# Kernel optimization log

Hardware: AMD Instinct MI355X
Metric: run time of the kernel (lower is better)

## Reference

```python
import jax, jax.numpy as jnp
import numpy as np

N = 50000
E = 1_600_000
HID = 128
NF = 128
NG = 64
CUTOFF = 10.0
LOG2 = float(np.log(2.0))
PI = float(np.pi)


def ssp(v):
    # ShiftedSoftplus: softplus(v) - log(2), numerically stable
    return jnp.logaddexp(v, 0.0) - LOG2


def setup_inputs() -> dict:
    key = jax.random.key(0)
    ks = jax.random.split(key, 12)
    s = 0.05
    x = jax.random.normal(ks[0], (N, HID), dtype=jnp.float32)
    edge_index = jax.random.randint(ks[1], (2, E), 0, N, dtype=jnp.int64 if jax.config.jax_enable_x64 else jnp.int32)
    edge_length = jax.random.uniform(ks[2], (E,), dtype=jnp.float32) * 12.0
    edge_attr = jax.random.normal(ks[3], (E, NG), dtype=jnp.float32)
    return {
        "x": x,
        "edge_index": edge_index,
        "edge_length": edge_length,
        "edge_attr": edge_attr,
        "lin1_w": jax.random.normal(ks[4], (HID, NF), dtype=jnp.float32) * s,
        "nn_w1": jax.random.normal(ks[5], (NG, NF), dtype=jnp.float32) * s,
        "nn_b1": jnp.zeros((NF,), dtype=jnp.float32),
        "nn_w2": jax.random.normal(ks[6], (NF, NF), dtype=jnp.float32) * s,
        "nn_b2": jnp.zeros((NF,), dtype=jnp.float32),
        "lin2_w": jax.random.normal(ks[7], (NF, HID), dtype=jnp.float32) * s,
        "lin2_b": jnp.zeros((HID,), dtype=jnp.float32),
        "lin_w": jax.random.normal(ks[8], (HID, HID), dtype=jnp.float32) * s,
        "lin_b": jnp.zeros((HID,), dtype=jnp.float32),
    }


def reference(x, edge_index, edge_length, edge_attr,
              lin1_w, nn_w1, nn_b1, nn_w2, nn_b2,
              lin2_w, lin2_b, lin_w, lin_b):
    # edge filter MLP: [E, NG] -> [E, NF]
    W = ssp(edge_attr @ nn_w1 + nn_b1) @ nn_w2 + nn_b2
    # cosine cutoff envelope
    C = 0.5 * (jnp.cos(edge_length * (PI / CUTOFF)) + 1.0)
    C = C * (edge_length <= CUTOFF) * (edge_length >= 0.0)
    W = W * C[:, None]
    # node projection, gather source, multiply, scatter-add to target
    h = x @ lin1_w                                   # [N, NF]
    src, dst = edge_index[0], edge_index[1]
    msg = h[src] * W                                 # [E, NF]
    agg = jax.ops.segment_sum(msg, dst, num_segments=N)  # [N, NF]
    out = agg @ lin2_w + lin2_b                      # [N, HID]
    out = ssp(out)
    out = out @ lin_w + lin_b
    return out
```

## Files before the change

kernel.cpp:

```cpp
#include <hip/hip_runtime.h>


typedef __attribute__((ext_vector_type(8))) short bf16x8;
typedef __attribute__((ext_vector_type(4))) float f32x4;

static __device__ __forceinline__ float sspf(float v) {
    return fmaxf(v, 0.0f) + __logf(1.0f + __expf(-fabsf(v))) - 0.69314718f;
}

static __device__ __forceinline__ short bf16s(float x) {
    unsigned u = __builtin_bit_cast(unsigned, x);
    return (short)((u + 0x7fffu + ((u >> 16) & 1u)) >> 16);
}

__global__ __launch_bounds__(256) void node_proj_kernel(
    const float* __restrict__ x, const float* __restrict__ w,
    float* __restrict__ h, int n)
{
    __shared__ float xsT[128 * 20];
    int row0 = blockIdx.x * 16;
    for (int i = threadIdx.x; i < 2048; i += 256) {
        int r = i >> 7, c = i & 127;
        int rr = row0 + r;
        xsT[c * 20 + r] = (rr < n) ? x[(size_t)rr * 128 + c] : 0.0f;
    }
    __syncthreads();
    int j = threadIdx.x & 127;
    int rb = (threadIdx.x >> 7) * 8;
    float acc[8] = {0, 0, 0, 0, 0, 0, 0, 0};
    for (int k = 0; k < 128; ++k) {
        float wk = w[k * 128 + j];
        const float4* xp = (const float4*)&xsT[k * 20 + rb];
        float4 u0 = xp[0], u1 = xp[1];
        acc[0] = fmaf(u0.x, wk, acc[0]);
        acc[1] = fmaf(u0.y, wk, acc[1]);
        acc[2] = fmaf(u0.z, wk, acc[2]);
        acc[3] = fmaf(u0.w, wk, acc[3]);
        acc[4] = fmaf(u1.x, wk, acc[4]);
        acc[5] = fmaf(u1.y, wk, acc[5]);
        acc[6] = fmaf(u1.z, wk, acc[6]);
        acc[7] = fmaf(u1.w, wk, acc[7]);
    }
#pragma unroll
    for (int r = 0; r < 8; ++r) {
        int rr = row0 + rb + r;
        if (rr < n) h[(size_t)rr * 128 + j] = acc[r];
    }
}

__global__ __launch_bounds__(512, 4) void edge_kernel(
    const float* __restrict__ eattr, const int* __restrict__ eidx,
    const float* __restrict__ elen,
    const float* __restrict__ w1, const float* __restrict__ b1,
    const float* __restrict__ w2, const float* __restrict__ b2,
    const float* __restrict__ h, float* __restrict__ agg, int E)
{
    __shared__ short w1T[128 * 72];
    __shared__ short w2T[128 * 136];
    __shared__ short tseg[8 * 16 * 40];

    for (int i = threadIdx.x; i < 64 * 128; i += 512) {
        int k = i >> 7, nn = i & 127;
        w1T[nn * 72 + k] = bf16s(w1[i]);
    }
    for (int i = threadIdx.x; i < 128 * 128; i += 512) {
        int k = i >> 7, nn = i & 127;
        w2T[nn * 136 + k] = bf16s(w2[i]);
    }
    __syncthreads();

    const int lane = threadIdx.x & 63;
    const int m = lane & 15;
    const int q = lane >> 4;
    short* tw = tseg + (threadIdx.x >> 6) * (16 * 40);

    float b1v[8], b2v[8];
#pragma unroll
    for (int u = 0; u < 8; ++u) {
        b1v[u] = b1[u * 16 + m];
        b2v[u] = b2[u * 16 + m];
    }

    const int ngroups = (E + 15) >> 4;
    int wid = blockIdx.x * 8 + (threadIdx.x >> 6);
    int stride = gridDim.x * 8;

    for (int g = wid; g < ngroups; g += stride) {
        int e0 = g << 4;

        int erow = e0 + m;
        if (erow >= E) erow = E - 1;
        const float* ap = eattr + (size_t)erow * 64 + q * 8;
        float4 x0 = *(const float4*)(ap);
        float4 x1 = *(const float4*)(ap + 4);
        float4 x2 = *(const float4*)(ap + 32);
        float4 x3 = *(const float4*)(ap + 36);
        bf16x8 af0, af1;
        af0[0] = bf16s(x0.x); af0[1] = bf16s(x0.y);
        af0[2] = bf16s(x0.z); af0[3] = bf16s(x0.w);
        af0[4] = bf16s(x1.x); af0[5] = bf16s(x1.y);
        af0[6] = bf16s(x1.z); af0[7] = bf16s(x1.w);
        af1[0] = bf16s(x2.x); af1[1] = bf16s(x2.y);
        af1[2] = bf16s(x2.z); af1[3] = bf16s(x2.w);
        af1[4] = bf16s(x3.x); af1[5] = bf16s(x3.y);
        af1[6] = bf16s(x3.z); af1[7] = bf16s(x3.w);

        float cvv[4];
        int sV[4], dV[4];
#pragma unroll
        for (int r = 0; r < 4; ++r) {
            int e = e0 + 4 * q + r;
            int ec = (e < E) ? e : 0;
            float len = elen[ec];
            sV[r] = eidx[ec];
            dV[r] = eidx[E + ec];
            bool ok = (e < E) && (len <= 10.0f) && (len >= 0.0f);
            cvv[r] = ok ? 0.5f * (__cosf(len * 0.31415927f) + 1.0f) : 0.0f;
        }

        f32x4 acc2[8];
#pragma unroll
        for (int nt = 0; nt < 8; ++nt) {
            f32x4 c; c[0] = b2v[nt]; c[1] = b2v[nt]; c[2] = b2v[nt]; c[3] = b2v[nt];
            acc2[nt] = c;
        }

#pragma unroll
        for (int k2 = 0; k2 < 4; ++k2) {
            f32x4 acc1[2];
#pragma unroll
            for (int t = 0; t < 2; ++t) {
                float bv = b1v[2 * k2 + t];
                f32x4 c; c[0] = bv; c[1] = bv; c[2] = bv; c[3] = bv;
                acc1[t] = c;
            }
#pragma unroll
            for (int t = 0; t < 2; ++t) {
#pragma unroll
                for (int a = 0; a < 2; ++a) {
                    bf16x8 bw = *(const bf16x8*)&w1T[(16 * (2 * k2 + t) + m) * 72 + a * 32 + q * 8];
                    acc1[t] = __builtin_amdgcn_mfma_f32_16x16x32_bf16(
                        (a == 0) ? af0 : af1, bw, acc1[t], 0, 0, 0);
                }
            }
#pragma unroll
            for (int t = 0; t < 2; ++t) {
#pragma unroll
                for (int r = 0; r < 4; ++r) {
                    tw[(4 * q + r) * 40 + 16 * t + m] = bf16s(sspf(acc1[t][r]));
                }
            }
            bf16x8 ta = *(const bf16x8*)&tw[m * 40 + q * 8];
#pragma unroll
            for (int nt = 0; nt < 8; ++nt) {
                bf16x8 bw2 = *(const bf16x8*)&w2T[(16 * nt + m) * 136 + k2 * 32 + q * 8];
                acc2[nt] = __builtin_amdgcn_mfma_f32_16x16x32_bf16(ta, bw2, acc2[nt], 0, 0, 0);
            }
        }

#pragma unroll
        for (int r = 0; r < 4; ++r) {
            float cv = cvv[r];
            if (cv != 0.0f) {
                const float* hp = h + (size_t)sV[r] * 128 + m;
                float* gp = agg + (size_t)dV[r] * 128 + m;
#pragma unroll
                for (int nt = 0; nt < 8; ++nt) {
                    float Wv = acc2[nt][r] * cv;
                    atomicAdd(gp + nt * 16, hp[nt * 16] * Wv);
                }
            }
        }
    }
}

__global__ __launch_bounds__(256) void out_kernel(
    const float* __restrict__ agg,
    const float* __restrict__ w2, const float* __restrict__ b2,
    const float* __restrict__ w3, const float* __restrict__ b3,
    float* __restrict__ out, int n)
{
    __shared__ float aT[128 * 20];
    __shared__ float mT[128 * 20];
    int row0 = blockIdx.x * 16;
    for (int i = threadIdx.x; i < 2048; i += 256) {
        int r = i >> 7, c = i & 127;
        int rr = row0 + r;
        aT[c * 20 + r] = (rr < n) ? agg[(size_t)rr * 128 + c] : 0.0f;
    }
    __syncthreads();
    int j = threadIdx.x & 127;
    int rb = (threadIdx.x >> 7) * 8;

    float acc[8];
    float bj = b2[j];
#pragma unroll
    for (int r = 0; r < 8; ++r) acc[r] = bj;
    for (int k = 0; k < 128; ++k) {
        float wk = w2[k * 128 + j];
        const float4* xp = (const float4*)&aT[k * 20 + rb];
        float4 u0 = xp[0], u1 = xp[1];
        acc[0] = fmaf(u0.x, wk, acc[0]);
        acc[1] = fmaf(u0.y, wk, acc[1]);
        acc[2] = fmaf(u0.z, wk, acc[2]);
        acc[3] = fmaf(u0.w, wk, acc[3]);
        acc[4] = fmaf(u1.x, wk, acc[4]);
        acc[5] = fmaf(u1.y, wk, acc[5]);
        acc[6] = fmaf(u1.z, wk, acc[6]);
        acc[7] = fmaf(u1.w, wk, acc[7]);
    }
    float4 s0, s1;
    s0.x = sspf(acc[0]); s0.y = sspf(acc[1]); s0.z = sspf(acc[2]); s0.w = sspf(acc[3]);
    s1.x = sspf(acc[4]); s1.y = sspf(acc[5]); s1.z = sspf(acc[6]); s1.w = sspf(acc[7]);
    ((float4*)&mT[j * 20 + rb])[0] = s0;
    ((float4*)&mT[j * 20 + rb])[1] = s1;
    __syncthreads();

    float bj3 = b3[j];
#pragma unroll
    for (int r = 0; r < 8; ++r) acc[r] = bj3;
    for (int k = 0; k < 128; ++k) {
        float wk = w3[k * 128 + j];
        const float4* xp = (const float4*)&mT[k * 20 + rb];
        float4 u0 = xp[0], u1 = xp[1];
        acc[0] = fmaf(u0.x, wk, acc[0]);
        acc[1] = fmaf(u0.y, wk, acc[1]);
        acc[2] = fmaf(u0.z, wk, acc[2]);
        acc[3] = fmaf(u0.w, wk, acc[3]);
        acc[4] = fmaf(u1.x, wk, acc[4]);
        acc[5] = fmaf(u1.y, wk, acc[5]);
        acc[6] = fmaf(u1.z, wk, acc[6]);
        acc[7] = fmaf(u1.w, wk, acc[7]);
    }
#pragma unroll
    for (int r = 0; r < 8; ++r) {
        int rr = row0 + rb + r;
        if (rr < n) out[(size_t)rr * 128 + j] = acc[r];
    }
}

extern "C" void kernel_launch(void* const* d_in, const int* in_sizes, int n_in,
                              void* d_out, int out_size, void* d_ws, size_t ws_size,
                              hipStream_t stream)
{
    const float* x     = (const float*)d_in[0];
    const int*   eidx  = (const int*)d_in[1];
    const float* elen  = (const float*)d_in[2];
    const float* eattr = (const float*)d_in[3];
    const float* lin1w = (const float*)d_in[4];
    const float* nnw1  = (const float*)d_in[5];
    const float* nnb1  = (const float*)d_in[6];
    const float* nnw2  = (const float*)d_in[7];
    const float* nnb2  = (const float*)d_in[8];
    const float* lin2w = (const float*)d_in[9];
    const float* lin2b = (const float*)d_in[10];
    const float* linw  = (const float*)d_in[11];
    const float* linb  = (const float*)d_in[12];

    int n = in_sizes[0] / 128;
    int E = in_sizes[2];

    float* h   = (float*)d_ws;
    float* agg = h + (size_t)n * 128;

    hipMemsetAsync(agg, 0, (size_t)n * 128 * sizeof(float), stream);

    node_proj_kernel<<<(n + 15) / 16, 256, 0, stream>>>(x, lin1w, h, n);
    edge_kernel<<<512, 512, 0, stream>>>(eattr, eidx, elen,
                                         nnw1, nnb1, nnw2, nnb2, h, agg, E);
    out_kernel<<<(n + 15) / 16, 256, 0, stream>>>(agg, lin2w, lin2b, linw, linb,
                                                  (float*)d_out, n);
}
```

Measured before the change: 1.248 ms.

## Transpose first edge MFMA and pass activations via shuffles instead of LDS

The first filter MFMA is swapped to compute the transposed tile, so the ssp activations can be packed to bf16 pairs and redistributed with wave shuffles. This replaces the per-wave LDS staging buffer. Biases move to shared memory and b2 is added at the scatter stage, which frees registers; occupancy is raised to 6 blocks of 512 with a 768-block grid. The node and output GEMM kernels also change their thread-to-column mapping to two columns by four rows. The extra shuffles and selects add ALU work, and the higher occupancy target may force register spills.

```diff
diff --git a/kernel.cpp b/kernel.cpp
--- a/kernel.cpp
+++ b/kernel.cpp
@@ -11,6 +11,10 @@
 static __device__ __forceinline__ short bf16s(float x) {
     unsigned u = __builtin_bit_cast(unsigned, x);
     return (short)((u + 0x7fffu + ((u >> 16) & 1u)) >> 16);
+}
+static __device__ __forceinline__ int packbf(float lo, float hi) {
+    return (int)(((unsigned)(unsigned short)bf16s(lo)) |
+                 (((unsigned)(unsigned short)bf16s(hi)) << 16));
 }
 
 __global__ __launch_bounds__(256) void node_proj_kernel(
@@ -25,30 +29,33 @@
         xsT[c * 20 + r] = (rr < n) ? x[(size_t)rr * 128 + c] : 0.0f;
     }
     __syncthreads();
-    int j = threadIdx.x & 127;
-    int rb = (threadIdx.x >> 7) * 8;
+    int c0 = threadIdx.x & 63, c1 = c0 + 64;
+    int rg = threadIdx.x >> 6;
     float acc[8] = {0, 0, 0, 0, 0, 0, 0, 0};
     for (int k = 0; k < 128; ++k) {
-        float wk = w[k * 128 + j];
-        const float4* xp = (const float4*)&xsT[k * 20 + rb];
-        float4 u0 = xp[0], u1 = xp[1];
-        acc[0] = fmaf(u0.x, wk, acc[0]);
-        acc[1] = fmaf(u0.y, wk, acc[1]);
-        acc[2] = fmaf(u0.z, wk, acc[2]);
-        acc[3] = fmaf(u0.w, wk, acc[3]);
-        acc[4] = fmaf(u1.x, wk, acc[4]);
-        acc[5] = fmaf(u1.y, wk, acc[5]);
-        acc[6] = fmaf(u1.z, wk, acc[6]);
-        acc[7] = fmaf(u1.w, wk, acc[7]);
-    }
-#pragma unroll
-    for (int r = 0; r < 8; ++r) {
-        int rr = row0 + rb + r;
-        if (rr < n) h[(size_t)rr * 128 + j] = acc[r];
-    }
-}
-
-__global__ __launch_bounds__(512, 4) void edge_kernel(
+        float4 xv = *(const float4*)&xsT[k * 20 + 4 * rg];
+        float w0 = w[k * 128 + c0];
+        float w1v = w[k * 128 + c1];
+        acc[0] = fmaf(xv.x, w0, acc[0]);
+        acc[1] = fmaf(xv.y, w0, acc[1]);
+        acc[2] = fmaf(xv.z, w0, acc[2]);
+        acc[3] = fmaf(xv.w, w0, acc[3]);
+        acc[4] = fmaf(xv.x, w1v, acc[4]);
+        acc[5] = fmaf(xv.y, w1v, acc[5]);
+        acc[6] = fmaf(xv.z, w1v, acc[6]);
+        acc[7] = fmaf(xv.w, w1v, acc[7]);
+    }
+#pragma unroll
+    for (int r = 0; r < 4; ++r) {
+        int rr = row0 + 4 * rg + r;
+        if (rr < n) {
+            h[(size_t)rr * 128 + c0] = acc[r];
+            h[(size_t)rr * 128 + c1] = acc[4 + r];
+        }
+    }
+}
+
+__global__ __launch_bounds__(512, 6) void edge_kernel(
     const float* __restrict__ eattr, const int* __restrict__ eidx,
     const float* __restrict__ elen,
     const float* __restrict__ w1, const float* __restrict__ b1,
@@ -57,29 +64,30 @@
 {
     __shared__ short w1T[128 * 72];
     __shared__ short w2T[128 * 136];
-    __shared__ short tseg[8 * 16 * 40];
+    __shared__ float b1s[128];
+    __shared__ float b2s[128];
 
     for (int i = threadIdx.x; i < 64 * 128; i += 512) {
-        int k = i >> 7, nn = i & 127;
-        w1T[nn * 72 + k] = bf16s(w1[i]);
+        int k = i >> 7, c = i & 127;
+        w1T[c * 72 + k] = bf16s(w1[i]);
     }
     for (int i = threadIdx.x; i < 128 * 128; i += 512) {
-        int k = i >> 7, nn = i & 127;
-        w2T[nn * 136 + k] = bf16s(w2[i]);
+        int k = i >> 7, c = i & 127;
+        w2T[c * 136 + k] = bf16s(w2[i]);
+    }
+    if (threadIdx.x < 128) {
+        b1s[threadIdx.x] = b1[threadIdx.x];
+        b2s[threadIdx.x] = b2[threadIdx.x];
     }
     __syncthreads();
 
     const int lane = threadIdx.x & 63;
     const int m = lane & 15;
     const int q = lane >> 4;
-    short* tw = tseg + (threadIdx.x >> 6) * (16 * 40);
-
-    float b1v[8], b2v[8];
-#pragma unroll
-    for (int u = 0; u < 8; ++u) {
-        b1v[u] = b1[u * 16 + m];
-        b2v[u] = b2[u * 16 + m];
-    }
+    const int s_ = q & 1;
+    const int L0 = 32 * s_ + m;
+    const int L1 = L0 + 16;
+    const bool hiTile = (q >= 2);
 
     const int ngroups = (E + 15) >> 4;
     int wid = blockIdx.x * 8 + (threadIdx.x >> 6);
@@ -105,6 +113,49 @@
         af1[4] = bf16s(x3.x); af1[5] = bf16s(x3.y);
         af1[6] = bf16s(x3.z); af1[7] = bf16s(x3.w);
 
+        f32x4 acc2[8];
+#pragma unroll
+        for (int nt = 0; nt < 8; ++nt) {
+            f32x4 z; z[0] = 0.f; z[1] = 0.f; z[2] = 0.f; z[3] = 0.f;
+            acc2[nt] = z;
+        }
+
+#pragma unroll
+        for (int kc = 0; kc < 4; ++kc) {
+            int pk[4];
+#pragma unroll
+            for (int t = 0; t < 2; ++t) {
+                int ct2 = 2 * kc + t;
+                f32x4 a1; a1[0] = 0.f; a1[1] = 0.f; a1[2] = 0.f; a1[3] = 0.f;
+                bf16x8 wA0 = *(const bf16x8*)&w1T[(16 * ct2 + m) * 72 + 8 * q];
+                bf16x8 wA1 = *(const bf16x8*)&w1T[(16 * ct2 + m) * 72 + 32 + 8 * q];
+                a1 = __builtin_amdgcn_mfma_f32_16x16x32_bf16(wA0, af0, a1, 0, 0, 0);
+                a1 = __builtin_amdgcn_mfma_f32_16x16x32_bf16(wA1, af1, a1, 0, 0, 0);
+                float4 bb = *(const float4*)&b1s[16 * ct2 + 4 * q];
+                float v0 = sspf(a1[0] + bb.x);
+                float v1 = sspf(a1[1] + bb.y);
+                float v2 = sspf(a1[2] + bb.z);
+                float v3 = sspf(a1[3] + bb.w);
+                pk[2 * t]     = packbf(v0, v1);
+                pk[2 * t + 1] = packbf(v2, v3);
+            }
+            int fa0 = __shfl(pk[0], L0), fa1 = __shfl(pk[1], L0);
+            int fa2 = __shfl(pk[0], L1), fa3 = __shfl(pk[1], L1);
+            int fb0 = __shfl(pk[2], L0), fb1 = __shfl(pk[3], L0);
+            int fb2 = __shfl(pk[2], L1), fb3 = __shfl(pk[3], L1);
+            int4 fr;
+            fr.x = hiTile ? fb0 : fa0;
+            fr.y = hiTile ? fb1 : fa1;
+            fr.z = hiTile ? fb2 : fa2;
+            fr.w = hiTile ? fb3 : fa3;
+            bf16x8 ta = __builtin_bit_cast(bf16x8, fr);
+#pragma unroll
+            for (int nt = 0; nt < 8; ++nt) {
+                bf16x8 bw2 = *(const bf16x8*)&w2T[(16 * nt + m) * 136 + 32 * kc + 8 * q];
+                acc2[nt] = __builtin_amdgcn_mfma_f32_16x16x32_bf16(ta, bw2, acc2[nt], 0, 0, 0);
+            }
+        }
+
         float cvv[4];
         int sV[4], dV[4];
 #pragma unroll
@@ -117,46 +168,9 @@
             bool ok = (e < E) && (len <= 10.0f) && (len >= 0.0f);
             cvv[r] = ok ? 0.5f * (__cosf(len * 0.31415927f) + 1.0f) : 0.0f;
         }
-
-        f32x4 acc2[8];
-#pragma unroll
-        for (int nt = 0; nt < 8; ++nt) {
-            f32x4 c; c[0] = b2v[nt]; c[1] = b2v[nt]; c[2] = b2v[nt]; c[3] = b2v[nt];
-            acc2[nt] = c;
-        }
-
-#pragma unroll
-        for (int k2 = 0; k2 < 4; ++k2) {
-            f32x4 acc1[2];
-#pragma unroll
-            for (int t = 0; t < 2; ++t) {
-                float bv = b1v[2 * k2 + t];
-                f32x4 c; c[0] = bv; c[1] = bv; c[2] = bv; c[3] = bv;
-                acc1[t] = c;
-            }
-#pragma unroll
-            for (int t = 0; t < 2; ++t) {
-#pragma unroll
-                for (int a = 0; a < 2; ++a) {
-                    bf16x8 bw = *(const bf16x8*)&w1T[(16 * (2 * k2 + t) + m) * 72 + a * 32 + q * 8];
-                    acc1[t] = __builtin_amdgcn_mfma_f32_16x16x32_bf16(
-                        (a == 0) ? af0 : af1, bw, acc1[t], 0, 0, 0);
-                }
-            }
-#pragma unroll
-            for (int t = 0; t < 2; ++t) {
-#pragma unroll
-                for (int r = 0; r < 4; ++r) {
-                    tw[(4 * q + r) * 40 + 16 * t + m] = bf16s(sspf(acc1[t][r]));
-                }
-            }
-            bf16x8 ta = *(const bf16x8*)&tw[m * 40 + q * 8];
-#pragma unroll
-            for (int nt = 0; nt < 8; ++nt) {
-                bf16x8 bw2 = *(const bf16x8*)&w2T[(16 * nt + m) * 136 + k2 * 32 + q * 8];
-                acc2[nt] = __builtin_amdgcn_mfma_f32_16x16x32_bf16(ta, bw2, acc2[nt], 0, 0, 0);
-            }
-        }
+        float b2l[8];
+#pragma unroll
+        for (int nt = 0; nt < 8; ++nt) b2l[nt] = b2s[16 * nt + m];
 
 #pragma unroll
         for (int r = 0; r < 4; ++r) {
@@ -166,7 +180,7 @@
                 float* gp = agg + (size_t)dV[r] * 128 + m;
 #pragma unroll
                 for (int nt = 0; nt < 8; ++nt) {
-                    float Wv = acc2[nt][r] * cv;
+                    float Wv = (acc2[nt][r] + b2l[nt]) * cv;
                     atomicAdd(gp + nt * 16, hp[nt * 16] * Wv);
                 }
             }
@@ -189,53 +203,56 @@
         aT[c * 20 + r] = (rr < n) ? agg[(size_t)rr * 128 + c] : 0.0f;
     }
     __syncthreads();
-    int j = threadIdx.x & 127;
-    int rb = (threadIdx.x >> 7) * 8;
+    int c0 = threadIdx.x & 63, c1 = c0 + 64;
+    int rg = threadIdx.x >> 6;
 
     float acc[8];
-    float bj = b2[j];
-#pragma unroll
-    for (int r = 0; r < 8; ++r) acc[r] = bj;
+    float b0 = b2[c0], b1v = b2[c1];
+#pragma unroll
+    for (int r = 0; r < 4; ++r) { acc[r] = b0; acc[4 + r] = b1v; }
     for (int k = 0; k < 128; ++k) {
-        float wk = w2[k * 128 + j];
-        const float4* xp = (const float4*)&aT[k * 20 + rb];
-        float4 u0 = xp[0], u1 = xp[1];
-        acc[0] = fmaf(u0.x, wk, acc[0]);
-        acc[1] = fmaf(u0.y, wk, acc[1]);
-        acc[2] = fmaf(u0.z, wk, acc[2]);
-        acc[3] = fmaf(u0.w, wk, acc[3]);
-        acc[4] = fmaf(u1.x, wk, acc[4]);
-        acc[5] = fmaf(u1.y, wk, acc[5]);
-        acc[6] = fmaf(u1.z, wk, acc[6]);
-        acc[7] = fmaf(u1.w, wk, acc[7]);
+        float4 xv = *(const float4*)&aT[k * 20 + 4 * rg];
+        float w0 = w2[k * 128 + c0];
+        float w1v = w2[k * 128 + c1];
+        acc[0] = fmaf(xv.x, w0, acc[0]);
+        acc[1] = fmaf(xv.y, w0, acc[1]);
+        acc[2] = fmaf(xv.z, w0, acc[2]);
+        acc[3] = fmaf(xv.w, w0, acc[3]);
+        acc[4] = fmaf(xv.x, w1v, acc[4]);
+        acc[5] = fmaf(xv.y, w1v, acc[5]);
+        acc[6] = fmaf(xv.z, w1v, acc[6]);
+        acc[7] = fmaf(xv.w, w1v, acc[7]);
     }
     float4 s0, s1;
     s0.x = sspf(acc[0]); s0.y = sspf(acc[1]); s0.z = sspf(acc[2]); s0.w = sspf(acc[3]);
     s1.x = sspf(acc[4]); s1.y = sspf(acc[5]); s1.z = sspf(acc[6]); s1.w = sspf(acc[7]);
-    ((float4*)&mT[j * 20 + rb])[0] = s0;
-    ((float4*)&mT[j * 20 + rb])[1] = s1;
-    __syncthreads();
-
-    float bj3 = b3[j];
-#pragma unroll
-    for (int r = 0; r < 8; ++r) acc[r] = bj3;
+    *(float4*)&mT[c0 * 20 + 4 * rg] = s0;
+    *(float4*)&mT[c1 * 20 + 4 * rg] = s1;
+    __syncthreads();
+
+    float b30 = b3[c0], b31 = b3[c1];
+#pragma unroll
+    for (int r = 0; r < 4; ++r) { acc[r] = b30; acc[4 + r] = b31; }
     for (int k = 0; k < 128; ++k) {
-        float wk = w3[k * 128 + j];
-        const float4* xp = (const float4*)&mT[k * 20 + rb];
-        float4 u0 = xp[0], u1 = xp[1];
-        acc[0] = fmaf(u0.x, wk, acc[0]);
-        acc[1] = fmaf(u0.y, wk, acc[1]);
-        acc[2] = fmaf(u0.z, wk, acc[2]);
-        acc[3] = fmaf(u0.w, wk, acc[3]);
-        acc[4] = fmaf(u1.x, wk, acc[4]);
-        acc[5] = fmaf(u1.y, wk, acc[5]);
-        acc[6] = fmaf(u1.z, wk, acc[6]);
-        acc[7] = fmaf(u1.w, wk, acc[7]);
-    }
-#pragma unroll
-    for (int r = 0; r < 8; ++r) {
-        int rr = row0 + rb + r;
-        if (rr < n) out[(size_t)rr * 128 + j] = acc[r];
+        float4 xv = *(const float4*)&mT[k * 20 + 4 * rg];
+        float w0 = w3[k * 128 + c0];
+        float w1v = w3[k * 128 + c1];
+        acc[0] = fmaf(xv.x, w0, acc[0]);
+        acc[1] = fmaf(xv.y, w0, acc[1]);
+        acc[2] = fmaf(xv.z, w0, acc[2]);
+        acc[3] = fmaf(xv.w, w0, acc[3]);
+        acc[4] = fmaf(xv.x, w1v, acc[4]);
+        acc[5] = fmaf(xv.y, w1v, acc[5]);
+        acc[6] = fmaf(xv.z, w1v, acc[6]);
+        acc[7] = fmaf(xv.w, w1v, acc[7]);
+    }
+#pragma unroll
+    for (int r = 0; r < 4; ++r) {
+        int rr = row0 + 4 * rg + r;
+        if (rr < n) {
+            out[(size_t)rr * 128 + c0] = acc[r];
+            out[(size_t)rr * 128 + c1] = acc[4 + r];
+        }
     }
 }
 
@@ -266,7 +283,7 @@
     hipMemsetAsync(agg, 0, (size_t)n * 128 * sizeof(float), stream);
 
     node_proj_kernel<<<(n + 15) / 16, 256, 0, stream>>>(x, lin1w, h, n);
-    edge_kernel<<<512, 512, 0, stream>>>(eattr, eidx, elen,
+    edge_kernel<<<768, 512, 0, stream>>>(eattr, eidx, elen,
                                          nnw1, nnb1, nnw2, nnb2, h, agg, E);
     out_kernel<<<(n + 15) / 16, 256, 0, stream>>>(agg, lin2w, lin2b, linw, linb,
                                                   (float*)d_out, n);
```

New measurement: 2.252 ms. 1.81x slower.
